# Optimization experiments

Hardware: AMD Instinct MI355X
Metric: run time of the kernel (lower is better)

The kernel has to match this reference:

```python
import jax, jax.numpy as jnp
import numpy as np

CPV = 64  # cpv_size; output_size = CPV*(CPV+1)//2 = 2080

def _tri_indices(cpv):
    # Reproduce the torch nested-loop scatter order:
    # for idx_x in range(cpv): for idx_y in range(cpv-idx_x): col = cpv-1-idx_y
    rows = np.repeat(np.arange(cpv), cpv - np.arange(cpv))
    cols = np.concatenate([np.arange(cpv - 1, i - 1, -1) for i in range(cpv)])
    return jnp.asarray(rows), jnp.asarray(cols)


def setup_inputs() -> dict:
    key = jax.random.key(0)
    ks = jax.random.split(key, 12)
    B, D_in, H, L = 8192, 1024, 2048, CPV * (CPV + 1) // 2
    s = lambda fan_in: 1.0 / np.sqrt(fan_in)
    return {
        "x":   jax.random.normal(ks[0], (B, D_in), jnp.float32),
        "W1":  jax.random.uniform(ks[1], (D_in, H), jnp.float32, -s(D_in), s(D_in)),
        "b1":  jnp.zeros((H,), jnp.float32),
        "W2":  jax.random.uniform(ks[2], (H, H), jnp.float32, -s(H), s(H)),
        "b2":  jnp.zeros((H,), jnp.float32),
        "W21": jax.random.uniform(ks[3], (H, H), jnp.float32, -s(H), s(H)),
        "b21": jnp.zeros((H,), jnp.float32),
        "W22": jax.random.uniform(ks[4], (H, H), jnp.float32, -s(H), s(H)),
        "b22": jnp.zeros((H,), jnp.float32),
        "W3":  jax.random.uniform(ks[5], (H, L), jnp.float32, -s(H), s(H)),
        "b3":  jnp.zeros((L,), jnp.float32),
    }


def reference(x, W1, b1, W2, b2, W21, b21, W22, b22, W3, b3):
    lrelu = lambda t: jax.nn.leaky_relu(t, 0.01)
    h = lrelu(x @ W1 + b1)
    h = lrelu(h @ W2 + b2)
    h = lrelu(h @ W21 + b21)
    h = lrelu(h @ W22 + b22)
    y = h @ W3 + b3  # [B, L] with L = CPV*(CPV+1)//2
    rows, cols = _tri_indices(CPV)
    is_diag = rows == cols  # diagonal entries are abs'ed (negated when <= 0)
    vals = jnp.where(is_diag[None, :] & (y <= 0), -y, y)
    B = y.shape[0]
    M = jnp.zeros((B, CPV, CPV), y.dtype).at[:, rows, cols].set(vals)
    return jnp.transpose(M, (1, 2, 0))  # torch stacks per-example matrices on dim=2
```

## Files before the change

kernel.cpp:

```cpp
#include <hip/hip_runtime.h>
#include <hip/hip_bf16.h>
#include <stdint.h>

typedef short short8  __attribute__((ext_vector_type(8)));
typedef float f32x4   __attribute__((ext_vector_type(4)));
typedef float f32x16  __attribute__((ext_vector_type(16)));

typedef __attribute__((address_space(1))) uint32_t u32_g;
typedef __attribute__((address_space(3))) uint32_t u32_l;

#define BM 128
#define BN 128
#define BK 64

__device__ __forceinline__ void gld_lds16(const void* g, const void* l) {
  __builtin_amdgcn_global_load_lds((u32_g*)(uintptr_t)g, (u32_l*)(uintptr_t)l, 16, 0, 0);
}

__global__ __launch_bounds__(256) void gemm32_k(
    const __hip_bfloat16* __restrict__ A,
    const __hip_bfloat16* __restrict__ BT,
    const float* __restrict__ bias,
    __hip_bfloat16* __restrict__ C,
    int K)
{
  __shared__ __attribute__((aligned(16))) __hip_bfloat16 As[BM * BK];
  __shared__ __attribute__((aligned(16))) __hip_bfloat16 Bs[BN * BK];

  const int tid  = threadIdx.x;
  const int lane = tid & 63;
  const int l31  = lane & 31;
  const int half = lane >> 5;
  const int wave = tid >> 6;
  const int wm   = (wave >> 1) << 6;
  const int wn   = (wave & 1) << 6;

  const int bm = blockIdx.x * BM;
  const int bn = blockIdx.y * BN;

  const __hip_bfloat16* ag[4];
  const __hip_bfloat16* bg[4];
  uint32_t lofs[4];
#pragma unroll
  for (int c = 0; c < 4; ++c) {
    int ci   = tid + 256 * c;
    int row  = ci >> 3;
    int chk  = ci & 7;
    int gchk = chk ^ (row & 7);
    ag[c]   = A  + (size_t)(bm + row) * K + gchk * 8;
    bg[c]   = BT + (size_t)(bn + row) * K + gchk * 8;
    lofs[c] = (uint32_t)ci * 16u;
  }

  f32x16 acc[2][2];
#pragma unroll
  for (int i = 0; i < 2; ++i)
#pragma unroll
    for (int j = 0; j < 2; ++j)
      acc[i][j] = (f32x16)(0.f);

  const int nk = K >> 6;
  for (int kt = 0; kt < nk; ++kt) {
#pragma unroll
    for (int c = 0; c < 4; ++c) {
      gld_lds16(ag[c], (const char*)As + lofs[c]);
      gld_lds16(bg[c], (const char*)Bs + lofs[c]);
      ag[c] += BK;
      bg[c] += BK;
    }
    __syncthreads();
#pragma unroll
    for (int kk = 0; kk < 4; ++kk) {
      short8 af[2], bf[2];
      const int cf = kk * 2 + half;
#pragma unroll
      for (int t = 0; t < 2; ++t) {
        int m  = wm + t * 32 + l31;
        af[t]  = *(const short8*)(As + m * BK + (cf ^ (m & 7)) * 8);
        int n  = wn + t * 32 + l31;
        bf[t]  = *(const short8*)(Bs + n * BK + (cf ^ (n & 7)) * 8);
      }
#pragma unroll
      for (int ti = 0; ti < 2; ++ti)
#pragma unroll
        for (int tj = 0; tj < 2; ++tj)
          acc[ti][tj] = __builtin_amdgcn_mfma_f32_32x32x16_bf16(af[ti], bf[tj], acc[ti][tj], 0, 0, 0);
    }
    __syncthreads();
  }

#pragma unroll
  for (int tj = 0; tj < 2; ++tj) {
    int   n  = bn + wn + tj * 32 + l31;
    float bv = bias[n];
#pragma unroll
    for (int ti = 0; ti < 2; ++ti) {
      int base = bm + wm + ti * 32 + 4 * half;
#pragma unroll
      for (int reg = 0; reg < 16; ++reg) {
        int m   = base + (reg & 3) + 8 * (reg >> 2);
        float v = acc[ti][tj][reg] + bv;
        v = (v > 0.f) ? v : 0.01f * v;
        C[(size_t)m * 2048 + n] = __float2bfloat16(v);
      }
    }
  }
}

__global__ __launch_bounds__(256) void gemm16f_k(
    const __hip_bfloat16* __restrict__ A,
    const __hip_bfloat16* __restrict__ BT,
    const float* __restrict__ bias,
    float* __restrict__ Cf,
    const int* __restrict__ tbl,
    int K, int Nreal)
{
  __shared__ __attribute__((aligned(16))) __hip_bfloat16 As[BM * BK];
  __shared__ __attribute__((aligned(16))) __hip_bfloat16 Bs[BN * BK];

  const int tid  = threadIdx.x;
  const int lane = tid & 63;
  const int l15  = lane & 15;
  const int quad = lane >> 4;
  const int wave = tid >> 6;
  const int wm   = (wave >> 1) << 6;
  const int wn   = (wave & 1) << 6;

  const int bm = blockIdx.x * BM;
  const int bn = blockIdx.y * BN;

  const __hip_bfloat16* ag[4];
  const __hip_bfloat16* bg[4];
  uint32_t lofs[4];
#pragma unroll
  for (int c = 0; c < 4; ++c) {
    int ci   = tid + 256 * c;
    int row  = ci >> 3;
    int chk  = ci & 7;
    int gchk = chk ^ (row & 7);
    ag[c]   = A  + (size_t)(bm + row) * K + gchk * 8;
    bg[c]   = BT + (size_t)(bn + row) * K + gchk * 8;
    lofs[c] = (uint32_t)ci * 16u;
  }

  f32x4 acc[4][4];
#pragma unroll
  for (int i = 0; i < 4; ++i)
#pragma unroll
    for (int j = 0; j < 4; ++j)
      acc[i][j] = (f32x4){0.f, 0.f, 0.f, 0.f};

  const int nk = K >> 6;
  for (int kt = 0; kt < nk; ++kt) {
#pragma unroll
    for (int c = 0; c < 4; ++c) {
      gld_lds16(ag[c], (const char*)As + lofs[c]);
      gld_lds16(bg[c], (const char*)Bs + lofs[c]);
      ag[c] += BK;
      bg[c] += BK;
    }
    __syncthreads();
#pragma unroll
    for (int ks = 0; ks < 2; ++ks) {
      short8 af[4], bf[4];
      const int cf = ks * 4 + quad;
#pragma unroll
      for (int i = 0; i < 4; ++i) {
        int m  = wm + i * 16 + l15;
        af[i]  = *(const short8*)(As + m * BK + ((cf ^ (m & 7)) * 8));
      }
#pragma unroll
      for (int j = 0; j < 4; ++j) {
        int n  = wn + j * 16 + l15;
        bf[j]  = *(const short8*)(Bs + n * BK + ((cf ^ (n & 7)) * 8));
      }
#pragma unroll
      for (int i = 0; i < 4; ++i)
#pragma unroll
        for (int j = 0; j < 4; ++j)
          acc[i][j] = __builtin_amdgcn_mfma_f32_16x16x32_bf16(af[i], bf[j], acc[i][j], 0, 0, 0);
    }
    __syncthreads();
  }

#pragma unroll
  for (int j = 0; j < 4; ++j) {
    int n = bn + wn + j * 16 + l15;
    if (n < Nreal) {
      float bv   = bias[n];
      int  code  = tbl[n];
      int  dst   = code & 4095;
      bool diag  = (code & 4096) != 0;
#pragma unroll
      for (int i = 0; i < 4; ++i) {
        int m0 = bm + wm + i * 16 + quad * 4;
        f32x4 pk;
#pragma unroll
        for (int r = 0; r < 4; ++r) {
          float v = acc[i][j][r] + bv;
          if (diag) v = fabsf(v);
          pk[r] = v;
        }
        *reinterpret_cast<f32x4*>(Cf + (size_t)dst * 8192 + m0) = pk;
      }
    }
  }
}

__global__ __launch_bounds__(256) void prep_k(
    const float* __restrict__ x,   __hip_bfloat16* __restrict__ xb,
    const float* __restrict__ W1,  __hip_bfloat16* __restrict__ W1T,
    const float* __restrict__ W2,  __hip_bfloat16* __restrict__ W2T,
    const float* __restrict__ W21, __hip_bfloat16* __restrict__ W21T,
    const float* __restrict__ W22, __hip_bfloat16* __restrict__ W22T,
    const float* __restrict__ W3,  __hip_bfloat16* __restrict__ W3T,
    float* __restrict__ out, int* __restrict__ tbl)
{
  __shared__ __hip_bfloat16 t[32][33];
  const int tid = threadIdx.x;
  int bid = blockIdx.x;

  if (bid < 8192) {
    int i = bid * 1024 + tid * 4;
    float4 v = *reinterpret_cast<const float4*>(x + i);
    union { unsigned short us[4]; uint2 v2; } pk;
    __hip_bfloat16 h;
    h = __float2bfloat16(v.x); pk.us[0] = *reinterpret_cast<unsigned short*>(&h);
    h = __float2bfloat16(v.y); pk.us[1] = *reinterpret_cast<unsigned short*>(&h);
    h = __float2bfloat16(v.z); pk.us[2] = *reinterpret_cast<unsigned short*>(&h);
    h = __float2bfloat16(v.w); pk.us[3] = *reinterpret_cast<unsigned short*>(&h);
    *reinterpret_cast<uint2*>(xb + i) = pk.v2;
    return;
  }
  bid -= 8192;

  if (bid < 18688) {
    const float* src; __hip_bfloat16* dst; int K, N, nbx, b;
    if (bid < 2048)       { src = W1;  dst = W1T;  K = 1024; N = 2048; nbx = 64; b = bid;         }
    else if (bid < 6144)  { src = W2;  dst = W2T;  K = 2048; N = 2048; nbx = 64; b = bid - 2048;  }
    else if (bid < 10240) { src = W21; dst = W21T; K = 2048; N = 2048; nbx = 64; b = bid - 6144;  }
    else if (bid < 14336) { src = W22; dst = W22T; K = 2048; N = 2048; nbx = 64; b = bid - 10240; }
    else                  { src = W3;  dst = W3T;  K = 2048; N = 2080; nbx = 68; b = bid - 14336; }
    const int bx = b % nbx, by = b / nbx;
    const int n0 = bx * 32, k0 = by * 32;
    const int tx = tid & 31, ty = tid >> 5;
    const __hip_bfloat16 zero = __float2bfloat16(0.f);
#pragma unroll
    for (int r = 0; r < 32; r += 8) {
      int k = k0 + ty + r, n = n0 + tx;
      t[ty + r][tx] = (n < N) ? __float2bfloat16(src[(size_t)k * N + n]) : zero;
    }
    __syncthreads();
#pragma unroll
    for (int r = 0; r < 32; r += 8) {
      int n = n0 + ty + r;
      dst[(size_t)n * K + k0 + tx] = t[tx][ty + r];
    }
    return;
  }
  bid -= 18688;

  if (bid < 2016) {
    int p = bid;
    int r = (int)((1.0f + sqrtf(1.0f + 8.0f * (float)p)) * 0.5f);
    while (r * (r - 1) / 2 > p) --r;
    while ((r + 1) * r / 2 <= p) ++r;
    int c = p - r * (r - 1) / 2;
    float* dstp = out + (size_t)(r * 64 + c) * 8192;
    f32x4 z = (f32x4){0.f, 0.f, 0.f, 0.f};
#pragma unroll
    for (int i = 0; i < 8; ++i)
      *reinterpret_cast<f32x4*>(dstp + i * 1024 + tid * 4) = z;
    return;
  }
  bid -= 2016;

  int l = bid * 256 + tid;
  if (l < 2080) {
    int r = 0, s = 0;
    while (s + (64 - r) <= l) { s += 64 - r; ++r; }
    int c = 63 - (l - s);
    tbl[l] = (r * 64 + c) | ((r == c) ? 4096 : 0);
  }
}

extern "C" void kernel_launch(void* const* d_in, const int* in_sizes, int n_in,
                              void* d_out, int out_size, void* d_ws, size_t ws_size,
                              hipStream_t stream)
{
  const float* x   = (const float*)d_in[0];
  const float* W1  = (const float*)d_in[1];
  const float* b1  = (const float*)d_in[2];
  const float* W2  = (const float*)d_in[3];
  const float* b2  = (const float*)d_in[4];
  const float* W21 = (const float*)d_in[5];
  const float* b21 = (const float*)d_in[6];
  const float* W22 = (const float*)d_in[7];
  const float* b22 = (const float*)d_in[8];
  const float* W3  = (const float*)d_in[9];
  const float* b3  = (const float*)d_in[10];
  float* out = (float*)d_out;

  char* ws = (char*)d_ws;
  __hip_bfloat16* act0 = (__hip_bfloat16*)(ws);
  __hip_bfloat16* act1 = (__hip_bfloat16*)(ws + ((size_t)32 << 20));
  __hip_bfloat16* xb   = act1;
  __hip_bfloat16* W1T  = (__hip_bfloat16*)(ws + ((size_t)64 << 20));
  __hip_bfloat16* W2T  = (__hip_bfloat16*)(ws + ((size_t)68 << 20));
  __hip_bfloat16* W21T = (__hip_bfloat16*)(ws + ((size_t)76 << 20));
  __hip_bfloat16* W22T = (__hip_bfloat16*)(ws + ((size_t)84 << 20));
  __hip_bfloat16* W3T  = (__hip_bfloat16*)(ws + ((size_t)92 << 20));
  int*            tbl  = (int*)(ws + ((size_t)101 << 20));

  prep_k<<<28905, 256, 0, stream>>>(x, xb, W1, W1T, W2, W2T, W21, W21T,
                                    W22, W22T, W3, W3T, out, tbl);

  gemm32_k<<<dim3(64, 16), 256, 0, stream>>>(xb,   W1T,  b1,  act0, 1024);
  gemm32_k<<<dim3(64, 16), 256, 0, stream>>>(act0, W2T,  b2,  act1, 2048);
  gemm32_k<<<dim3(64, 16), 256, 0, stream>>>(act1, W21T, b21, act0, 2048);
  gemm32_k<<<dim3(64, 16), 256, 0, stream>>>(act0, W22T, b22, act1, 2048);
  gemm16f_k<<<dim3(64, 17), 256, 0, stream>>>(act1, W3T, b3, out, tbl, 2048, 2080);
}
```

Before: 633.1 us.

## Overlap weight transposes and output zeroing with preceding GEMM launches

New measurement: 651.4 us. 2.9% more time.

```diff
diff --git a/kernel.cpp b/kernel.cpp
--- a/kernel.cpp
+++ b/kernel.cpp
@@ -15,6 +15,42 @@
 
 __device__ __forceinline__ void gld_lds16(const void* g, const void* l) {
   __builtin_amdgcn_global_load_lds((u32_g*)(uintptr_t)g, (u32_l*)(uintptr_t)l, 16, 0, 0);
+}
+
+
+__device__ __forceinline__ void aux_transpose(
+    __hip_bfloat16 (*t)[33],
+    const float* __restrict__ src, __hip_bfloat16* __restrict__ dst,
+    int K, int N, int nbx, int b, int tid)
+{
+  const int bx = b % nbx, by = b / nbx;
+  const int n0 = bx * 32, k0 = by * 32;
+  const int tx = tid & 31, ty = tid >> 5;
+  const __hip_bfloat16 zero = __float2bfloat16(0.f);
+#pragma unroll
+  for (int r = 0; r < 32; r += 8) {
+    int k = k0 + ty + r, n = n0 + tx;
+    t[ty + r][tx] = (n < N) ? __float2bfloat16(src[(size_t)k * N + n]) : zero;
+  }
+  __syncthreads();
+#pragma unroll
+  for (int r = 0; r < 32; r += 8) {
+    int n = n0 + ty + r;
+    dst[(size_t)n * K + k0 + tx] = t[tx][ty + r];
+  }
+}
+
+__device__ __forceinline__ void aux_zlo(float* __restrict__ out, int p, int tid)
+{
+  int r = (int)((1.0f + sqrtf(1.0f + 8.0f * (float)p)) * 0.5f);
+  while (r * (r - 1) / 2 > p) --r;
+  while ((r + 1) * r / 2 <= p) ++r;
+  int c = p - r * (r - 1) / 2;
+  float* dstp = out + (size_t)(r * 64 + c) * 8192;
+  f32x4 z = (f32x4){0.f, 0.f, 0.f, 0.f};
+#pragma unroll
+  for (int i = 0; i < 8; ++i)
+    *reinterpret_cast<f32x4*>(dstp + i * 1024 + tid * 4) = z;
 }
 
 __global__ __launch_bounds__(256) void gemm32_k(
@@ -22,12 +58,28 @@
     const __hip_bfloat16* __restrict__ BT,
     const float* __restrict__ bias,
     __hip_bfloat16* __restrict__ C,
-    int K)
+    int K,
+    const float* __restrict__ tsrc, __hip_bfloat16* __restrict__ tdst,
+    int tK, int tN, int tnbx, int tblocks,
+    float* __restrict__ zout, int zstart, int zcount)
 {
   __shared__ __attribute__((aligned(16))) __hip_bfloat16 As[BM * BK];
   __shared__ __attribute__((aligned(16))) __hip_bfloat16 Bs[BN * BK];
 
-  const int tid  = threadIdx.x;
+  const int tid = threadIdx.x;
+  const int bid = blockIdx.x;
+
+  if (bid >= 1024) {
+    int a = bid - 1024;
+    if (a < tblocks) {
+      aux_transpose(reinterpret_cast<__hip_bfloat16(*)[33]>(As),
+                    tsrc, tdst, tK, tN, tnbx, a, tid);
+    } else {
+      aux_zlo(zout, zstart + (a - tblocks), tid);
+    }
+    return;
+  }
+
   const int lane = tid & 63;
   const int l31  = lane & 31;
   const int half = lane >> 5;
@@ -35,8 +87,8 @@
   const int wm   = (wave >> 1) << 6;
   const int wn   = (wave & 1) << 6;
 
-  const int bm = blockIdx.x * BM;
-  const int bn = blockIdx.y * BN;
+  const int bm = (bid & 63) * BM;
+  const int bn = (bid >> 6) * BN;
 
   const __hip_bfloat16* ag[4];
   const __hip_bfloat16* bg[4];
@@ -126,8 +178,9 @@
   const int wm   = (wave >> 1) << 6;
   const int wn   = (wave & 1) << 6;
 
-  const int bm = blockIdx.x * BM;
-  const int bn = blockIdx.y * BN;
+  const int bid = blockIdx.x;
+  const int bm = (bid & 63) * BM;
+  const int bn = (bid >> 6) * BN;
 
   const __hip_bfloat16* ag[4];
   const __hip_bfloat16* bg[4];
@@ -208,13 +261,9 @@
 }
 
 __global__ __launch_bounds__(256) void prep_k(
-    const float* __restrict__ x,   __hip_bfloat16* __restrict__ xb,
-    const float* __restrict__ W1,  __hip_bfloat16* __restrict__ W1T,
-    const float* __restrict__ W2,  __hip_bfloat16* __restrict__ W2T,
-    const float* __restrict__ W21, __hip_bfloat16* __restrict__ W21T,
-    const float* __restrict__ W22, __hip_bfloat16* __restrict__ W22T,
-    const float* __restrict__ W3,  __hip_bfloat16* __restrict__ W3T,
-    float* __restrict__ out, int* __restrict__ tbl)
+    const float* __restrict__ x,  __hip_bfloat16* __restrict__ xb,
+    const float* __restrict__ W1, __hip_bfloat16* __restrict__ W1T,
+    int* __restrict__ tbl)
 {
   __shared__ __hip_bfloat16 t[32][33];
   const int tid = threadIdx.x;
@@ -234,46 +283,11 @@
   }
   bid -= 8192;
 
-  if (bid < 18688) {
-    const float* src; __hip_bfloat16* dst; int K, N, nbx, b;
-    if (bid < 2048)       { src = W1;  dst = W1T;  K = 1024; N = 2048; nbx = 64; b = bid;         }
-    else if (bid < 6144)  { src = W2;  dst = W2T;  K = 2048; N = 2048; nbx = 64; b = bid - 2048;  }
-    else if (bid < 10240) { src = W21; dst = W21T; K = 2048; N = 2048; nbx = 64; b = bid - 6144;  }
-    else if (bid < 14336) { src = W22; dst = W22T; K = 2048; N = 2048; nbx = 64; b = bid - 10240; }
-    else                  { src = W3;  dst = W3T;  K = 2048; N = 2080; nbx = 68; b = bid - 14336; }
-    const int bx = b % nbx, by = b / nbx;
-    const int n0 = bx * 32, k0 = by * 32;
-    const int tx = tid & 31, ty = tid >> 5;
-    const __hip_bfloat16 zero = __float2bfloat16(0.f);
-#pragma unroll
-    for (int r = 0; r < 32; r += 8) {
-      int k = k0 + ty + r, n = n0 + tx;
-      t[ty + r][tx] = (n < N) ? __float2bfloat16(src[(size_t)k * N + n]) : zero;
-    }
-    __syncthreads();
-#pragma unroll
-    for (int r = 0; r < 32; r += 8) {
-      int n = n0 + ty + r;
-      dst[(size_t)n * K + k0 + tx] = t[tx][ty + r];
-    }
+  if (bid < 2048) {
+    aux_transpose(t, W1, W1T, 1024, 2048, 64, bid, tid);
     return;
   }
-  bid -= 18688;
-
-  if (bid < 2016) {
-    int p = bid;
-    int r = (int)((1.0f + sqrtf(1.0f + 8.0f * (float)p)) * 0.5f);
-    while (r * (r - 1) / 2 > p) --r;
-    while ((r + 1) * r / 2 <= p) ++r;
-    int c = p - r * (r - 1) / 2;
-    float* dstp = out + (size_t)(r * 64 + c) * 8192;
-    f32x4 z = (f32x4){0.f, 0.f, 0.f, 0.f};
-#pragma unroll
-    for (int i = 0; i < 8; ++i)
-      *reinterpret_cast<f32x4*>(dstp + i * 1024 + tid * 4) = z;
-    return;
-  }
-  bid -= 2016;
+  bid -= 2048;
 
   int l = bid * 256 + tid;
   if (l < 2080) {
@@ -312,12 +326,23 @@
   __hip_bfloat16* W3T  = (__hip_bfloat16*)(ws + ((size_t)92 << 20));
   int*            tbl  = (int*)(ws + ((size_t)101 << 20));
 
-  prep_k<<<28905, 256, 0, stream>>>(x, xb, W1, W1T, W2, W2T, W21, W21T,
-                                    W22, W22T, W3, W3T, out, tbl);
-
-  gemm32_k<<<dim3(64, 16), 256, 0, stream>>>(xb,   W1T,  b1,  act0, 1024);
-  gemm32_k<<<dim3(64, 16), 256, 0, stream>>>(act0, W2T,  b2,  act1, 2048);
-  gemm32_k<<<dim3(64, 16), 256, 0, stream>>>(act1, W21T, b21, act0, 2048);
-  gemm32_k<<<dim3(64, 16), 256, 0, stream>>>(act0, W22T, b22, act1, 2048);
-  gemm16f_k<<<dim3(64, 17), 256, 0, stream>>>(act1, W3T, b3, out, tbl, 2048, 2080);
-}
+  prep_k<<<10249, 256, 0, stream>>>(x, xb, W1, W1T, tbl);
+
+  gemm32_k<<<1024 + 4096 + 1000, 256, 0, stream>>>(
+      xb, W1T, b1, act0, 1024,
+      W2, W2T, 2048, 2048, 64, 4096, out, 0, 1000);
+
+  gemm32_k<<<1024 + 4096 + 1016, 256, 0, stream>>>(
+      act0, W2T, b2, act1, 2048,
+      W21, W21T, 2048, 2048, 64, 4096, out, 1000, 1016);
+
+  gemm32_k<<<1024 + 4096, 256, 0, stream>>>(
+      act1, W21T, b21, act0, 2048,
+      W22, W22T, 2048, 2048, 64, 4096, out, 0, 0);
+
+  gemm32_k<<<1024 + 4352, 256, 0, stream>>>(
+      act0, W22T, b22, act1, 2048,
+      W3, W3T, 2048, 2080, 68, 4352, out, 0, 0);
+
+  gemm16f_k<<<64 * 17, 256, 0, stream>>>(act1, W3T, b3, out, tbl, 2048, 2080);
+}
```
